# Optimization experiments

Hardware: AMD Instinct MI355X
Metric: run time of the kernel (lower is better)

## Reference

```python
import jax, jax.numpy as jnp
import numpy as np

B, H = 8192, 2048


def setup_inputs() -> dict:
    key = jax.random.key(0)
    ks = jax.random.split(key, 8)
    s = 1.0 / np.sqrt(H)  # keep pre-activations in a sane range
    return {
        "x": jax.random.normal(ks[0], (B, H), dtype=jnp.float32),
        "ht": jax.random.normal(ks[1], (B, H), dtype=jnp.float32),
        "Wz": jax.random.normal(ks[2], (H, H), dtype=jnp.float32) * s,
        "Uz": jax.random.normal(ks[3], (H, H), dtype=jnp.float32) * s,
        "bz": jnp.zeros((H,), dtype=jnp.float32),
        "Wr": jax.random.normal(ks[4], (H, H), dtype=jnp.float32) * s,
        "Ur": jax.random.normal(ks[5], (H, H), dtype=jnp.float32) * s,
        "br": jnp.zeros((H,), dtype=jnp.float32),
        "Wh": jax.random.normal(ks[6], (H, H), dtype=jnp.float32) * s,
        "Uh": jax.random.normal(ks[7], (H, H), dtype=jnp.float32) * s,
        "bh": jnp.zeros((H,), dtype=jnp.float32),
    }


def reference(x, ht, Wz, Uz, bz, Wr, Ur, br, Wh, Uh, bh):
    # Fuse the three input-side GEMMs and the two state-side gate GEMMs.
    xz, xr, xh = jnp.split(x @ jnp.concatenate([Wz, Wr, Wh], axis=1), 3, axis=-1)
    hz, hr = jnp.split(ht @ jnp.concatenate([Uz, Ur], axis=1), 2, axis=-1)
    z = jax.nn.sigmoid(xz + hz + bz)
    r = jax.nn.sigmoid(xr + hr + br)
    h_tilde = jnp.tanh(xh + (r * ht) @ Uh + bh)
    new_state = (1.0 - z) * ht + z * h_tilde
    return new_state
```

## Files before the change

### kernel.cpp

```cpp
#include <hip/hip_runtime.h>
#include <hip/hip_bf16.h>

typedef unsigned short u16;
typedef __attribute__((ext_vector_type(4))) float f32x4;
typedef __attribute__((ext_vector_type(8))) short bf16x8;
typedef __attribute__((ext_vector_type(4))) unsigned short u16x4;

#define HDIM 2048
#define BM 128
#define BN 128
#define BK 32

__device__ __forceinline__ u16 f2bf(float f) {
  union { float f; unsigned u; } v; v.f = f;
  unsigned r = v.u + 0x7FFFu + ((v.u >> 16) & 1u);
  return (u16)(r >> 16);
}
__device__ __forceinline__ float bf2f(u16 h) {
  union { unsigned u; float f; } v; v.u = ((unsigned)h) << 16;
  return v.f;
}

__device__ __forceinline__ void gload_lds16(const u16* g, void* l) {
  __builtin_amdgcn_global_load_lds(
      (const __attribute__((address_space(1))) unsigned*)g,
      (__attribute__((address_space(3))) unsigned*)l, 16, 0, 0);
}

__global__ __launch_bounds__(256) void cast_bf(const float* __restrict__ x,
                                               const float* __restrict__ ht,
                                               u16* __restrict__ xb,
                                               u16* __restrict__ hb) {
  const int N4 = 8192 * HDIM / 4;
  int idx = blockIdx.x * 256 + threadIdx.x;
  const float* s;
  u16* d;
  int i;
  if (idx < N4) { s = x; d = xb; i = idx; }
  else          { s = ht; d = hb; i = idx - N4; }
  f32x4 v = *(const f32x4*)(s + (size_t)i * 4);
  u16x4 o;
  o.x = f2bf(v.x); o.y = f2bf(v.y); o.z = f2bf(v.z); o.w = f2bf(v.w);
  *(u16x4*)(d + (size_t)i * 4) = o;
}

__global__ __launch_bounds__(256) void transpose_cast(const float* __restrict__ src,
                                                      u16* __restrict__ dst, int dst_ld) {
  __shared__ float tile[32][33];
  int tx = threadIdx.x & 31, ty = threadIdx.x >> 5;
  int n0 = blockIdx.x * 32, k0 = blockIdx.y * 32;
#pragma unroll
  for (int i = 0; i < 32; i += 8)
    tile[ty + i][tx] = src[(size_t)(k0 + ty + i) * HDIM + n0 + tx];
  __syncthreads();
#pragma unroll
  for (int i = 0; i < 32; i += 8)
    dst[(size_t)(n0 + ty + i) * dst_ld + k0 + tx] = f2bf(tile[tx][ty + i]);
}

template <int EPI>
__global__ __launch_bounds__(256) void gemm2(
    const u16* __restrict__ A0, const u16* __restrict__ A1,
    const u16* __restrict__ Bt, int ldb, int K,
    const float* __restrict__ bias0,
    const float* __restrict__ bias1,
    const float* __restrict__ htp,
    float* __restrict__ zout,
    u16* __restrict__ o_a,
    float* __restrict__ o_final)
{
  __shared__ __attribute__((aligned(16))) char lds[2 * 16384];
  const int t = threadIdx.x;
  const int lane = t & 63;
  const int w = t >> 6;
  const int wr = w >> 1, wc = w & 1;
  const int m0 = blockIdx.y * BM;
  const int n0 = blockIdx.x * BN;
  const int K0 = K / 2;

  f32x4 acc[4][4];
#pragma unroll
  for (int i = 0; i < 4; ++i)
#pragma unroll
    for (int j = 0; j < 4; ++j)
      acc[i][j] = (f32x4){0.f, 0.f, 0.f, 0.f};

  const int sr = t >> 2;
  const int sc = t & 3;
  const int cs1 = sc ^ ((sr >> 1) & 3);
  const int cs2 = sc ^ (((sr + 64) >> 1) & 3);

  auto stage = [&](int buf, int k0) {
    const u16* Ap = (k0 < K0) ? A0 : A1;
    int kk = (k0 < K0) ? k0 : (k0 - K0);
    char* base = lds + buf * 16384;
    gload_lds16(Ap + (size_t)(m0 + sr) * K0 + kk + cs1 * 8, base + t * 16);
    gload_lds16(Ap + (size_t)(m0 + sr + 64) * K0 + kk + cs2 * 8, base + 4096 + t * 16);
    char* bb = base + 8192;
    gload_lds16(Bt + (size_t)(n0 + sr) * ldb + k0 + cs1 * 8, bb + t * 16);
    gload_lds16(Bt + (size_t)(n0 + sr + 64) * ldb + k0 + cs2 * 8, bb + 4096 + t * 16);
  };

  const int NT = K / BK;
  stage(0, 0);
  __syncthreads();
  int cur = 0;
  const int lrow = lane & 15;
  const int khi = lane >> 4;

  for (int tt = 0; tt < NT; ++tt) {
    if (tt + 1 < NT) stage(cur ^ 1, (tt + 1) * BK);
    const char* ab = lds + cur * 16384;
    const char* bb = ab + 8192;
    bf16x8 af[4], bfv[4];
#pragma unroll
    for (int mi = 0; mi < 4; ++mi) {
      int r = wr * 64 + mi * 16 + lrow;
      int off = r * 64 + ((khi ^ ((r >> 1) & 3)) * 16);
      af[mi] = *(const bf16x8*)(ab + off);
    }
#pragma unroll
    for (int ni = 0; ni < 4; ++ni) {
      int r = wc * 64 + ni * 16 + lrow;
      int off = r * 64 + ((khi ^ ((r >> 1) & 3)) * 16);
      bfv[ni] = *(const bf16x8*)(bb + off);
    }
#pragma unroll
    for (int mi = 0; mi < 4; ++mi)
#pragma unroll
      for (int ni = 0; ni < 4; ++ni)
        acc[mi][ni] = __builtin_amdgcn_mfma_f32_16x16x32_bf16(af[mi], bfv[ni], acc[mi][ni], 0, 0, 0);
    __syncthreads();
    cur ^= 1;
  }

  const int rbase = (lane >> 4) * 4;
  const int cbase = lane & 15;
#pragma unroll
  for (int mi = 0; mi < 4; ++mi) {
#pragma unroll
    for (int ni = 0; ni < 4; ++ni) {
#pragma unroll
      for (int j = 0; j < 4; ++j) {
        int row = m0 + wr * 64 + mi * 16 + rbase + j;
        int col = n0 + wc * 64 + ni * 16 + cbase;
        float v = acc[mi][ni][j];
        if constexpr (EPI == 1) {
          if (col < HDIM) {
            float zv = 1.f / (1.f + __expf(-(v + bias0[col])));
            zout[(size_t)row * HDIM + col] = zv;
          } else {
            int c = col - HDIM;
            float rv = 1.f / (1.f + __expf(-(v + bias1[c])));
            o_a[(size_t)row * HDIM + c] = f2bf(rv * htp[(size_t)row * HDIM + c]);
          }
        } else {
          float hv = tanhf(v + bias0[col]);
          float zv = zout[(size_t)row * HDIM + col];
          float hold = htp[(size_t)row * HDIM + col];
          o_final[(size_t)row * HDIM + col] = (1.f - zv) * hold + zv * hv;
        }
      }
    }
  }
}

extern "C" void kernel_launch(void* const* d_in, const int* in_sizes, int n_in,
                              void* d_out, int out_size, void* d_ws, size_t ws_size,
                              hipStream_t stream) {
  const float* x  = (const float*)d_in[0];
  const float* ht = (const float*)d_in[1];
  const float* Wz = (const float*)d_in[2];
  const float* Uz = (const float*)d_in[3];
  const float* bz = (const float*)d_in[4];
  const float* Wr = (const float*)d_in[5];
  const float* Ur = (const float*)d_in[6];
  const float* br = (const float*)d_in[7];
  const float* Wh = (const float*)d_in[8];
  const float* Uh = (const float*)d_in[9];
  const float* bh = (const float*)d_in[10];
  float* out = (float*)d_out;

  char* ws = (char*)d_ws;
  u16* xbf   = (u16*)(ws);
  u16* htbf  = (u16*)(ws + (((size_t)32) << 20));
  u16* abf   = (u16*)(ws + (((size_t)64) << 20));
  u16* bzrt  = (u16*)(ws + (((size_t)96) << 20));
  u16* whuht = (u16*)(ws + (((size_t)128) << 20));

  cast_bf<<<dim3(2 * 8192 * HDIM / 4 / 256), 256, 0, stream>>>(x, ht, xbf, htbf);

  dim3 tgrid(64, 64);
  transpose_cast<<<tgrid, 256, 0, stream>>>(Wz, bzrt, 4096);
  transpose_cast<<<tgrid, 256, 0, stream>>>(Uz, bzrt + 2048, 4096);
  transpose_cast<<<tgrid, 256, 0, stream>>>(Wr, bzrt + (size_t)2048 * 4096, 4096);
  transpose_cast<<<tgrid, 256, 0, stream>>>(Ur, bzrt + (size_t)2048 * 4096 + 2048, 4096);
  transpose_cast<<<tgrid, 256, 0, stream>>>(Wh, whuht, 4096);
  transpose_cast<<<tgrid, 256, 0, stream>>>(Uh, whuht + 2048, 4096);

  gemm2<1><<<dim3(32, 64), 256, 0, stream>>>(xbf, htbf, bzrt, 4096, 4096,
      bz, br, ht, out, abf, nullptr);

  gemm2<2><<<dim3(16, 64), 256, 0, stream>>>(xbf, abf, whuht, 4096, 4096,
      bh, nullptr, ht, out, nullptr, out);
}
```

Measured before the change: 910.2 us.

## Use 256x256 GEMM tiles with 8 waves, ping-pong LDS pipeline and block swizzle

Replaces the 128x128x32 GEMM with a 256x256x64 tile run by 512 threads (8 waves, each owning 128x64). The K tile is split into four quarter-loads that are interleaved with MFMA phases, with explicit vmcnt waits, barriers and s_setprio. Blocks are swizzled so neighbouring blocks share operand rows, and the six weight transposes are merged into a single launch. The aim is more data reuse per LDS byte and better overlap of loads with compute. In exchange it needs 128KB of LDS per block and much higher register pressure, which may limit occupancy.

```diff
diff --git a/kernel.cpp b/kernel.cpp
--- a/kernel.cpp
+++ b/kernel.cpp
@@ -7,9 +7,6 @@
 typedef __attribute__((ext_vector_type(4))) unsigned short u16x4;
 
 #define HDIM 2048
-#define BM 128
-#define BN 128
-#define BK 32
 
 __device__ __forceinline__ u16 f2bf(float f) {
   union { float f; unsigned u; } v; v.f = f;
@@ -20,11 +17,13 @@
   union { unsigned u; float f; } v; v.u = ((unsigned)h) << 16;
   return v.f;
 }
-
 __device__ __forceinline__ void gload_lds16(const u16* g, void* l) {
   __builtin_amdgcn_global_load_lds(
       (const __attribute__((address_space(1))) unsigned*)g,
       (__attribute__((address_space(3))) unsigned*)l, 16, 0, 0);
+}
+__device__ __forceinline__ f32x4 mfma16(bf16x8 a, bf16x8 b, f32x4 c) {
+  return __builtin_amdgcn_mfma_f32_16x16x32_bf16(a, b, c, 0, 0, 0);
 }
 
 __global__ __launch_bounds__(256) void cast_bf(const float* __restrict__ x,
@@ -33,9 +32,7 @@
                                                u16* __restrict__ hb) {
   const int N4 = 8192 * HDIM / 4;
   int idx = blockIdx.x * 256 + threadIdx.x;
-  const float* s;
-  u16* d;
-  int i;
+  const float* s; u16* d; int i;
   if (idx < N4) { s = x; d = xb; i = idx; }
   else          { s = ht; d = hb; i = idx - N4; }
   f32x4 v = *(const f32x4*)(s + (size_t)i * 4);
@@ -44,9 +41,22 @@
   *(u16x4*)(d + (size_t)i * 4) = o;
 }
 
-__global__ __launch_bounds__(256) void transpose_cast(const float* __restrict__ src,
-                                                      u16* __restrict__ dst, int dst_ld) {
+__global__ __launch_bounds__(256) void transpose_cast6(
+    const float* __restrict__ Wz, const float* __restrict__ Uz,
+    const float* __restrict__ Wr, const float* __restrict__ Ur,
+    const float* __restrict__ Wh, const float* __restrict__ Uh,
+    u16* __restrict__ bzrt, u16* __restrict__ whuht) {
   __shared__ float tile[32][33];
+  int z = blockIdx.z;
+  const float* src; u16* dst;
+  switch (z) {
+    case 0: src = Wz; dst = bzrt; break;
+    case 1: src = Uz; dst = bzrt + 2048; break;
+    case 2: src = Wr; dst = bzrt + (size_t)2048 * 4096; break;
+    case 3: src = Ur; dst = bzrt + (size_t)2048 * 4096 + 2048; break;
+    case 4: src = Wh; dst = whuht; break;
+    default: src = Uh; dst = whuht + 2048; break;
+  }
   int tx = threadIdx.x & 31, ty = threadIdx.x >> 5;
   int n0 = blockIdx.x * 32, k0 = blockIdx.y * 32;
 #pragma unroll
@@ -55,95 +65,152 @@
   __syncthreads();
 #pragma unroll
   for (int i = 0; i < 32; i += 8)
-    dst[(size_t)(n0 + ty + i) * dst_ld + k0 + tx] = f2bf(tile[tx][ty + i]);
+    dst[(size_t)(n0 + ty + i) * 4096 + k0 + tx] = f2bf(tile[tx][ty + i]);
 }
 
 template <int EPI>
-__global__ __launch_bounds__(256) void gemm2(
-    const u16* __restrict__ A0, const u16* __restrict__ A1,
-    const u16* __restrict__ Bt, int ldb, int K,
-    const float* __restrict__ bias0,
-    const float* __restrict__ bias1,
+__global__ __launch_bounds__(512, 2) void gemm8p(
+    const u16* __restrict__ A0g, const u16* __restrict__ A1g,
+    const u16* __restrict__ Btg,
+    const float* __restrict__ bias0, const float* __restrict__ bias1,
     const float* __restrict__ htp,
-    float* __restrict__ zout,
-    u16* __restrict__ o_a,
-    float* __restrict__ o_final)
+    float* zout, u16* __restrict__ o_a, float* o_final)
 {
-  __shared__ __attribute__((aligned(16))) char lds[2 * 16384];
+  __shared__ __attribute__((aligned(16))) char lds[131072];
+  const int K = 4096, K0 = 2048, NT = 64;
   const int t = threadIdx.x;
   const int lane = t & 63;
   const int w = t >> 6;
-  const int wr = w >> 1, wc = w & 1;
-  const int m0 = blockIdx.y * BM;
-  const int n0 = blockIdx.x * BN;
-  const int K0 = K / 2;
-
-  f32x4 acc[4][4];
-#pragma unroll
-  for (int i = 0; i < 4; ++i)
-#pragma unroll
-    for (int j = 0; j < 4; ++j)
-      acc[i][j] = (f32x4){0.f, 0.f, 0.f, 0.f};
-
-  const int sr = t >> 2;
-  const int sc = t & 3;
-  const int cs1 = sc ^ ((sr >> 1) & 3);
-  const int cs2 = sc ^ (((sr + 64) >> 1) & 3);
-
-  auto stage = [&](int buf, int k0) {
-    const u16* Ap = (k0 < K0) ? A0 : A1;
-    int kk = (k0 < K0) ? k0 : (k0 - K0);
-    char* base = lds + buf * 16384;
-    gload_lds16(Ap + (size_t)(m0 + sr) * K0 + kk + cs1 * 8, base + t * 16);
-    gload_lds16(Ap + (size_t)(m0 + sr + 64) * K0 + kk + cs2 * 8, base + 4096 + t * 16);
-    char* bb = base + 8192;
-    gload_lds16(Bt + (size_t)(n0 + sr) * ldb + k0 + cs1 * 8, bb + t * 16);
-    gload_lds16(Bt + (size_t)(n0 + sr + 64) * ldb + k0 + cs2 * 8, bb + 4096 + t * 16);
+  const int wm = w >> 2, wn = w & 3;
+
+  int nwg = gridDim.x;
+  int bid = blockIdx.x;
+  int swz = (bid & 7) * (nwg >> 3) + (bid >> 3);
+  const int m0 = (swz & 31) * 256;
+  const int n0 = (swz >> 5) * 256;
+
+  const int rowT = t >> 2;
+  const int srcChunk = (t & 3) ^ ((t >> 3) & 3);
+  const int dstOff = t * 16;
+
+  const int lrow = lane & 15;
+  const int khi_l = lane >> 4;
+  const int chunk = khi_l ^ ((lrow >> 1) & 3);
+  const int abase = wm * 8192 + lrow * 64 + chunk * 16;
+  const int bbase = wn * 4096 + lrow * 64 + chunk * 16;
+
+  f32x4 acc[8][4];
+#pragma unroll
+  for (int i = 0; i < 8; ++i)
+#pragma unroll
+    for (int j = 0; j < 4; ++j) acc[i][j] = (f32x4){0.f, 0.f, 0.f, 0.f};
+
+  auto issueHalf = [&](char* bufbase, int kt, int sub) {
+    int kbase = kt * 64 + (sub & 1) * 32 + srcChunk * 8;
+    char* dst = bufbase + sub * 16384 + dstOff;
+    if (sub < 2) {
+      const u16* Ap = A0g; int kk = kbase;
+      if (kbase >= K0) { Ap = A1g; kk = kbase - K0; }
+      gload_lds16(Ap + (size_t)(m0 + rowT) * K0 + kk, dst);
+      gload_lds16(Ap + (size_t)(m0 + 128 + rowT) * K0 + kk, dst + 8192);
+    } else {
+      gload_lds16(Btg + (size_t)(n0 + rowT) * K + kbase, dst);
+      gload_lds16(Btg + (size_t)(n0 + 128 + rowT) * K + kbase, dst + 8192);
+    }
   };
 
-  const int NT = K / BK;
-  stage(0, 0);
-  __syncthreads();
-  int cur = 0;
-  const int lrow = lane & 15;
-  const int khi = lane >> 4;
-
-  for (int tt = 0; tt < NT; ++tt) {
-    if (tt + 1 < NT) stage(cur ^ 1, (tt + 1) * BK);
-    const char* ab = lds + cur * 16384;
-    const char* bb = ab + 8192;
-    bf16x8 af[4], bfv[4];
-#pragma unroll
-    for (int mi = 0; mi < 4; ++mi) {
-      int r = wr * 64 + mi * 16 + lrow;
-      int off = r * 64 + ((khi ^ ((r >> 1) & 3)) * 16);
-      af[mi] = *(const bf16x8*)(ab + off);
-    }
-#pragma unroll
-    for (int ni = 0; ni < 4; ++ni) {
-      int r = wc * 64 + ni * 16 + lrow;
-      int off = r * 64 + ((khi ^ ((r >> 1) & 3)) * 16);
-      bfv[ni] = *(const bf16x8*)(bb + off);
-    }
-#pragma unroll
-    for (int mi = 0; mi < 4; ++mi)
-#pragma unroll
-      for (int ni = 0; ni < 4; ++ni)
-        acc[mi][ni] = __builtin_amdgcn_mfma_f32_16x16x32_bf16(af[mi], bfv[ni], acc[mi][ni], 0, 0, 0);
-    __syncthreads();
-    cur ^= 1;
+  issueHalf(lds, 0, 0); issueHalf(lds, 0, 2);
+  issueHalf(lds, 0, 1); issueHalf(lds, 0, 3);
+  asm volatile("s_waitcnt vmcnt(4)" ::: "memory");
+  __builtin_amdgcn_s_barrier();
+
+  bf16x8 Af[8], B0f[2], B1f[2], B2f[2], B3f[2];
+  {
+    const char* Bklo = lds + 32768;
+    B0f[0] = *(const bf16x8*)(Bklo + bbase);
+    B0f[1] = *(const bf16x8*)(Bklo + bbase + 1024);
+  }
+
+  for (int kt = 0; kt < NT; ++kt) {
+    char* curb = lds + (kt & 1) * 65536;
+    char* nxtb = lds + (((kt & 1) ^ 1)) * 65536;
+    const char* Aklo = curb;
+    const char* Akhi = curb + 16384;
+    const char* Bklo = curb + 32768;
+    const char* Bkhi = curb + 49152;
+    const bool pf = (kt + 1 < NT);
+
+    if (pf) issueHalf(nxtb, kt + 1, 0);
+#pragma unroll
+    for (int mi = 0; mi < 8; ++mi)
+      Af[mi] = *(const bf16x8*)(Aklo + abase + mi * 1024);
+    B1f[0] = *(const bf16x8*)(Bklo + bbase + 2048);
+    B1f[1] = *(const bf16x8*)(Bklo + bbase + 3072);
+    __builtin_amdgcn_s_setprio(1);
+#pragma unroll
+    for (int mi = 0; mi < 8; ++mi) {
+      acc[mi][0] = mfma16(Af[mi], B0f[0], acc[mi][0]);
+      acc[mi][1] = mfma16(Af[mi], B0f[1], acc[mi][1]);
+    }
+    __builtin_amdgcn_s_setprio(0);
+    if (pf) { asm volatile("s_waitcnt vmcnt(2)" ::: "memory"); }
+    else    { asm volatile("s_waitcnt vmcnt(0)" ::: "memory"); }
+    __builtin_amdgcn_s_barrier();
+
+    if (pf) issueHalf(nxtb, kt + 1, 2);
+    B2f[0] = *(const bf16x8*)(Bkhi + bbase);
+    B2f[1] = *(const bf16x8*)(Bkhi + bbase + 1024);
+    __builtin_amdgcn_s_setprio(1);
+#pragma unroll
+    for (int mi = 0; mi < 8; ++mi) {
+      acc[mi][2] = mfma16(Af[mi], B1f[0], acc[mi][2]);
+      acc[mi][3] = mfma16(Af[mi], B1f[1], acc[mi][3]);
+    }
+    __builtin_amdgcn_s_setprio(0);
+    __builtin_amdgcn_s_barrier();
+
+    if (pf) issueHalf(nxtb, kt + 1, 1);
+#pragma unroll
+    for (int mi = 0; mi < 8; ++mi)
+      Af[mi] = *(const bf16x8*)(Akhi + abase + mi * 1024);
+    B3f[0] = *(const bf16x8*)(Bkhi + bbase + 2048);
+    B3f[1] = *(const bf16x8*)(Bkhi + bbase + 3072);
+    __builtin_amdgcn_s_setprio(1);
+#pragma unroll
+    for (int mi = 0; mi < 8; ++mi) {
+      acc[mi][0] = mfma16(Af[mi], B2f[0], acc[mi][0]);
+      acc[mi][1] = mfma16(Af[mi], B2f[1], acc[mi][1]);
+    }
+    __builtin_amdgcn_s_setprio(0);
+    asm volatile("s_waitcnt vmcnt(2)" ::: "memory");
+    __builtin_amdgcn_s_barrier();
+
+    if (pf) issueHalf(nxtb, kt + 1, 3);
+    if (pf) {
+      const char* BkloN = nxtb + 32768;
+      B0f[0] = *(const bf16x8*)(BkloN + bbase);
+      B0f[1] = *(const bf16x8*)(BkloN + bbase + 1024);
+    }
+    __builtin_amdgcn_s_setprio(1);
+#pragma unroll
+    for (int mi = 0; mi < 8; ++mi) {
+      acc[mi][2] = mfma16(Af[mi], B3f[0], acc[mi][2]);
+      acc[mi][3] = mfma16(Af[mi], B3f[1], acc[mi][3]);
+    }
+    __builtin_amdgcn_s_setprio(0);
+    __builtin_amdgcn_s_barrier();
   }
 
   const int rbase = (lane >> 4) * 4;
   const int cbase = lane & 15;
 #pragma unroll
-  for (int mi = 0; mi < 4; ++mi) {
+  for (int mi = 0; mi < 8; ++mi) {
 #pragma unroll
     for (int ni = 0; ni < 4; ++ni) {
 #pragma unroll
       for (int j = 0; j < 4; ++j) {
-        int row = m0 + wr * 64 + mi * 16 + rbase + j;
-        int col = n0 + wc * 64 + ni * 16 + cbase;
+        int row = m0 + wm * 128 + mi * 16 + rbase + j;
+        int col = n0 + wn * 64 + ni * 16 + cbase;
         float v = acc[mi][ni][j];
         if constexpr (EPI == 1) {
           if (col < HDIM) {
@@ -190,17 +257,12 @@
 
   cast_bf<<<dim3(2 * 8192 * HDIM / 4 / 256), 256, 0, stream>>>(x, ht, xbf, htbf);
 
-  dim3 tgrid(64, 64);
-  transpose_cast<<<tgrid, 256, 0, stream>>>(Wz, bzrt, 4096);
-  transpose_cast<<<tgrid, 256, 0, stream>>>(Uz, bzrt + 2048, 4096);
-  transpose_cast<<<tgrid, 256, 0, stream>>>(Wr, bzrt + (size_t)2048 * 4096, 4096);
-  transpose_cast<<<tgrid, 256, 0, stream>>>(Ur, bzrt + (size_t)2048 * 4096 + 2048, 4096);
-  transpose_cast<<<tgrid, 256, 0, stream>>>(Wh, whuht, 4096);
-  transpose_cast<<<tgrid, 256, 0, stream>>>(Uh, whuht + 2048, 4096);
-
-  gemm2<1><<<dim3(32, 64), 256, 0, stream>>>(xbf, htbf, bzrt, 4096, 4096,
+  transpose_cast6<<<dim3(64, 64, 6), 256, 0, stream>>>(Wz, Uz, Wr, Ur, Wh, Uh,
+                                                       bzrt, whuht);
+
+  gemm8p<1><<<dim3(512), 512, 0, stream>>>(xbf, htbf, bzrt,
       bz, br, ht, out, abf, nullptr);
 
-  gemm2<2><<<dim3(16, 64), 256, 0, stream>>>(xbf, abf, whuht, 4096, 4096,
+  gemm8p<2><<<dim3(256), 512, 0, stream>>>(xbf, abf, whuht,
       bh, nullptr, ht, out, nullptr, out);
 }
```

After: 878.2 us. 3.5% less time.
